# Kernel tuning notes

Measured on AMD Instinct MI355X. Metric: run time of the kernel, lower is better.

Reference implementation:

```python
import jax, jax.numpy as jnp
import numpy as np

B, P, F = 128, 196, 2048   # batch, num_pixels, feature_dim
E, H, V = 512, 512, 10000  # embed_dim, hidden_dim, vocab_size
T = 32                     # max caption length


def setup_inputs() -> dict:
    key = jax.random.key(0)
    ks = jax.random.split(key, 12)
    s_e, s_h, s_f = 1.0 / np.sqrt(E), 1.0 / np.sqrt(H), 1.0 / np.sqrt(F)
    return {
        "features": jax.random.normal(ks[0], (B, P, F), jnp.float32),
        "captions": jax.random.randint(ks[1], (B, T), 0, V),
        # embedding table (init uniform(-0.1, 0.1) in the original)
        "emb_W": jax.random.uniform(ks[2], (V, E), jnp.float32, -0.1, 0.1),
        # LSTMCell params (PyTorch layout: [4H, in] with gate order i,f,g,o)
        "W_ih": jax.random.uniform(ks[3], (4 * H, E), jnp.float32, -s_h, s_h),
        "W_hh": jax.random.uniform(ks[4], (4 * H, H), jnp.float32, -s_h, s_h),
        "b_ih": jax.random.uniform(ks[5], (4 * H,), jnp.float32, -s_h, s_h),
        "b_hh": jax.random.uniform(ks[6], (4 * H,), jnp.float32, -s_h, s_h),
        # init_h / init_c linear layers: feature_dim -> hidden_dim
        "Wh": jax.random.uniform(ks[7], (H, F), jnp.float32, -s_f, s_f),
        "bh": jax.random.uniform(ks[8], (H,), jnp.float32, -s_f, s_f),
        "Wc": jax.random.uniform(ks[9], (H, F), jnp.float32, -s_f, s_f),
        "bc": jax.random.uniform(ks[10], (H,), jnp.float32, -s_f, s_f),
        # output projection (uniform(-0.1, 0.1) weights, zero bias)
        "fc_W": jax.random.uniform(ks[11], (V, H), jnp.float32, -0.1, 0.1),
        "fc_b": jnp.zeros((V,), jnp.float32),
    }


def _decode(features, captions, emb_W, W_ih, W_hh, b_ih, b_hh, Wh, bh, Wc, bc, fc_W, fc_b):
    # init hidden state from mean pooled features
    mean_feat = features.mean(axis=1)                       # [B, F]
    h0 = mean_feat @ Wh.T + bh                              # [B, H]
    c0 = mean_feat @ Wc.T + bc                              # [B, H]

    embeds = emb_W[captions]                                # [B, T, E]
    # x-side gate preactivations for all steps at once: [T-1, B, 4H]
    x_gates = jnp.einsum('bte,ge->tbg', embeds[:, :-1, :], W_ih) + (b_ih + b_hh)

    def step(carry, xg):
        h, c = carry
        gates = xg + h @ W_hh.T                             # [B, 4H]
        i, f, g, o = jnp.split(gates, 4, axis=-1)
        i, f, o = jax.nn.sigmoid(i), jax.nn.sigmoid(f), jax.nn.sigmoid(o)
        g = jnp.tanh(g)
        c_new = f * c + i * g
        h_new = o * jnp.tanh(c_new)
        return (h_new, c_new), h_new

    _, hs = jax.lax.scan(step, (h0, c0), x_gates)           # hs: [T-1, B, H]
    hs = jnp.swapaxes(hs, 0, 1)                             # [B, T-1, H]
    # dropout is identity in eval mode; fc applied per step == batched matmul
    return jnp.einsum('bth,vh->btv', hs, fc_W) + fc_b       # [B, T-1, V]


def reference(features, captions, emb_W, W_ih, W_hh, b_ih, b_hh, Wh, bh, Wc, bc, fc_W, fc_b):
    return _decode(features, captions, emb_W, W_ih, W_hh, b_ih, b_hh, Wh, bh, Wc, bc, fc_W, fc_b)
```

## Files before the change

kernel.cpp:

```cpp
#include <hip/hip_runtime.h>
#include <hip/hip_bf16.h>
#include <cstddef>

#define Bz 128
#define Pz 196
#define Fz 2048
#define Ez 512
#define Hz 512
#define Vz 10000
#define Tz 32
#define TM 31
#define Mrows (Bz * TM)
#define G4 (4 * Hz)
#define NPAD 10112

typedef __attribute__((ext_vector_type(8))) short bf16x8;
typedef __attribute__((ext_vector_type(4))) float f32x4;

__device__ __forceinline__ void gload_lds16(const void* g, void* l) {
    __builtin_amdgcn_global_load_lds(
        (const __attribute__((address_space(1))) unsigned int*)g,
        (__attribute__((address_space(3))) unsigned int*)l, 16, 0, 0);
}
__device__ __forceinline__ ushort f2b(float x) {
    __hip_bfloat16 b = __float2bfloat16(x);
    return *reinterpret_cast<ushort*>(&b);
}
__device__ __forceinline__ float b2f(ushort u) {
    __hip_bfloat16 b = *reinterpret_cast<__hip_bfloat16*>(&u);
    return __bfloat162float(b);
}

__global__ __launch_bounds__(256) void meanpool(const float* __restrict__ feat,
                                                float* __restrict__ mean) {
    int idx = blockIdx.x * 256 + threadIdx.x;
    int b = idx >> 9;
    int q = idx & 511;
    const float4* base = reinterpret_cast<const float4*>(feat) +
                         (size_t)b * Pz * (Fz / 4) + q;
    float4 acc = {0.f, 0.f, 0.f, 0.f};
    for (int p = 0; p < Pz; ++p) {
        float4 v = base[(size_t)p * (Fz / 4)];
        acc.x += v.x; acc.y += v.y; acc.z += v.z; acc.w += v.w;
    }
    const float s = 1.0f / (float)Pz;
    acc.x *= s; acc.y *= s; acc.z *= s; acc.w *= s;
    reinterpret_cast<float4*>(mean)[idx] = acc;
}

__global__ __launch_bounds__(256) void gather_cvt_emb(const float* __restrict__ emb,
                                                      const int* __restrict__ cap,
                                                      ushort* __restrict__ out) {
    int idx = blockIdx.x * 256 + threadIdx.x;
    if (idx >= Mrows * (Ez / 4)) return;
    int m = idx >> 7, kq = idx & 127;
    int b = m / TM;
    int t = m - b * TM;
    int row = cap[b * Tz + t];
    float4 v = reinterpret_cast<const float4*>(emb + (size_t)row * Ez)[kq];
    ushort4 o = {f2b(v.x), f2b(v.y), f2b(v.z), f2b(v.w)};
    reinterpret_cast<ushort4*>(out + (size_t)m * Ez)[kq] = o;
}

__global__ __launch_bounds__(256) void permute_wih(const float* __restrict__ W,
                                                   const float* __restrict__ b1,
                                                   const float* __restrict__ b2,
                                                   ushort* __restrict__ WP,
                                                   float* __restrict__ bP) {
    int idx = blockIdx.x * 256 + threadIdx.x;
    int o = idx >> 7, kq = idx & 127;
    int j = o >> 2, g = o & 3;
    int in = g * Hz + j;
    float4 v = reinterpret_cast<const float4*>(W + (size_t)in * Ez)[kq];
    ushort4 u = {f2b(v.x), f2b(v.y), f2b(v.z), f2b(v.w)};
    reinterpret_cast<ushort4*>(WP + (size_t)o * Ez)[kq] = u;
    if (kq == 0) bP[o] = b1[in] + b2[in];
}

__global__ __launch_bounds__(256) void permute_whh(const float* __restrict__ W,
                                                   ushort* __restrict__ Whi) {
    int idx = blockIdx.x * 256 + threadIdx.x;
    int o = idx >> 7, kq = idx & 127;
    int j = o >> 2, g = o & 3;
    int in = g * Hz + j;
    float4 v = reinterpret_cast<const float4*>(W + (size_t)in * Hz)[kq];
    ushort4 h = {f2b(v.x), f2b(v.y), f2b(v.z), f2b(v.w)};
    reinterpret_cast<ushort4*>(Whi + (size_t)o * Hz)[kq] = h;
}

__global__ __launch_bounds__(256) void cvt_bf16_pad4(const float* __restrict__ s,
                                                     ushort* __restrict__ d,
                                                     int n4src, int n4dst) {
    int i = blockIdx.x * 256 + threadIdx.x;
    if (i >= n4dst) return;
    ushort4 o;
    if (i < n4src) {
        float4 v = reinterpret_cast<const float4*>(s)[i];
        o.x = f2b(v.x); o.y = f2b(v.y); o.z = f2b(v.z); o.w = f2b(v.w);
    } else {
        o.x = o.y = o.z = o.w = 0;
    }
    reinterpret_cast<ushort4*>(d)[i] = o;
}

__global__ __launch_bounds__(256) void initk(
    const float* __restrict__ mean,
    const float* __restrict__ Wh, const float* __restrict__ Wc,
    float* __restrict__ partial)
{
    __shared__ float As[64][33];
    __shared__ float Bs2[64][33];
    const int n0 = blockIdx.x * 64;
    const int m0 = blockIdx.y * 64;
    const int kz = blockIdx.z;
    const int tid = threadIdx.x;
    const int tx = tid & 15, ty = tid >> 4;
    float acc[4][4] = {};

    for (int k0 = kz * 256; k0 < kz * 256 + 256; k0 += 32) {
#pragma unroll
        for (int i = 0; i < 2; ++i) {
            int e  = tid + i * 256;
            int r  = e >> 3;
            int cc = (e & 7) << 2;
            float4 va = *reinterpret_cast<const float4*>(
                mean + (size_t)(m0 + r) * Fz + k0 + cc);
            As[r][cc + 0] = va.x; As[r][cc + 1] = va.y;
            As[r][cc + 2] = va.z; As[r][cc + 3] = va.w;
            int n = n0 + r;
            const float* Brow = (n < Hz) ? (Wh + (size_t)n * Fz)
                                         : (Wc + (size_t)(n - Hz) * Fz);
            float4 vb = *reinterpret_cast<const float4*>(Brow + k0 + cc);
            Bs2[r][cc + 0] = vb.x; Bs2[r][cc + 1] = vb.y;
            Bs2[r][cc + 2] = vb.z; Bs2[r][cc + 3] = vb.w;
        }
        __syncthreads();
#pragma unroll
        for (int kk = 0; kk < 32; ++kk) {
            float a[4], bb[4];
#pragma unroll
            for (int i = 0; i < 4; ++i) a[i] = As[ty * 4 + i][kk];
#pragma unroll
            for (int j = 0; j < 4; ++j) bb[j] = Bs2[tx * 4 + j][kk];
#pragma unroll
            for (int i = 0; i < 4; ++i)
#pragma unroll
                for (int j = 0; j < 4; ++j)
                    acc[i][j] += a[i] * bb[j];
        }
        __syncthreads();
    }
#pragma unroll
    for (int i = 0; i < 4; ++i)
#pragma unroll
        for (int j = 0; j < 4; ++j)
            partial[((size_t)kz * 128 + m0 + ty * 4 + i) * 1024 + n0 + tx * 4 + j]
                = acc[i][j];
}

__global__ __launch_bounds__(256) void init_reduce(
    const float* __restrict__ partial,
    const float* __restrict__ bh, const float* __restrict__ bc,
    ushort* __restrict__ haHi, ushort* __restrict__ haLo,
    float* __restrict__ c0f)
{
    int idx = blockIdx.x * 256 + threadIdx.x;
    if (idx >= 128 * 1024) return;
    int m = idx >> 10, n = idx & 1023;
    float s = 0.f;
#pragma unroll
    for (int z = 0; z < 8; ++z)
        s += partial[((size_t)z * 128 + m) * 1024 + n];
    if (n < Hz) {
        s += bh[n];
        ushort hh = f2b(s);
        haHi[(size_t)m * Hz + n] = hh;
        haLo[(size_t)m * Hz + n] = f2b(s - b2f(hh));
    } else {
        c0f[(size_t)m * Hz + (n - Hz)] = s + bc[n - Hz];
    }
}

__global__ __launch_bounds__(256) void gemm_mfma(
    const ushort* __restrict__ A,
    const ushort* __restrict__ B,
    const float* __restrict__ bias,
    float* __restrict__ C,
    int Nb, int ldc, int K)
{
    __shared__ short Al[2][128 * 32];
    __shared__ short Bl[2][128 * 32];
    const int tid  = threadIdx.x;
    const int w    = tid >> 6;
    const int lane = tid & 63;

    const int nwg  = gridDim.x * gridDim.y;
    int orig = blockIdx.y * gridDim.x + blockIdx.x;
    int q = nwg >> 3, r = nwg & 7;
    int xcd = orig & 7, local = orig >> 3;
    int wgid = (xcd < r ? xcd * (q + 1) : r * (q + 1) + (xcd - r) * q) + local;
    const int m0 = (wgid / gridDim.x) * 128;
    const int n0 = (wgid % gridDim.x) * 128;
    const int wr = w >> 1, wc = w & 1;

    f32x4 acc[4][4] = {};

    const int srow = w * 32 + (lane >> 2);
    const int scol = (lane & 3) * 16;
    const char* Ag = (const char*)(A + (size_t)(m0 + srow) * K) + scol;
    const char* Bg = (const char*)(B + (size_t)(n0 + srow) * K) + scol;
    const size_t rstep = (size_t)16 * K * 2;
    const int ldsb = (w * 32) * 32;

    const int ko = (lane >> 4) * 8;
    const int fr = lane & 15;
    const int nk = K >> 5;

    {
        gload_lds16(Ag,         Al[0] + ldsb);
        gload_lds16(Ag + rstep, Al[0] + ldsb + 16 * 32);
        gload_lds16(Bg,         Bl[0] + ldsb);
        gload_lds16(Bg + rstep, Bl[0] + ldsb + 16 * 32);
    }
    __syncthreads();

    int cur = 0;
    for (int k = 0; k < nk; ++k) {
        if (k + 1 < nk) {
            const size_t kb = (size_t)(k + 1) * 64;
            gload_lds16(Ag + kb,         Al[cur ^ 1] + ldsb);
            gload_lds16(Ag + kb + rstep, Al[cur ^ 1] + ldsb + 16 * 32);
            gload_lds16(Bg + kb,         Bl[cur ^ 1] + ldsb);
            gload_lds16(Bg + kb + rstep, Bl[cur ^ 1] + ldsb + 16 * 32);
        }
        bf16x8 af[4], bf[4];
#pragma unroll
        for (int i = 0; i < 4; ++i)
            af[i] = *reinterpret_cast<const bf16x8*>(&Al[cur][(wr * 64 + i * 16 + fr) * 32 + ko]);
#pragma unroll
        for (int j = 0; j < 4; ++j)
            bf[j] = *reinterpret_cast<const bf16x8*>(&Bl[cur][(wc * 64 + j * 16 + fr) * 32 + ko]);
#pragma unroll
        for (int i = 0; i < 4; ++i)
#pragma unroll
            for (int j = 0; j < 4; ++j)
                acc[i][j] = __builtin_amdgcn_mfma_f32_16x16x32_bf16(
                    af[i], bf[j], acc[i][j], 0, 0, 0);
        __syncthreads();
        cur ^= 1;
    }

    const int r0 = (lane >> 4) * 4;
#pragma unroll
    for (int i = 0; i < 4; ++i) {
        int row = m0 + wr * 64 + i * 16 + r0;
#pragma unroll
        for (int j = 0; j < 4; ++j) {
            int col = n0 + wc * 64 + j * 16 + fr;
            if (col < Nb) {
                float bb = bias ? bias[col] : 0.f;
#pragma unroll
                for (int rr = 0; rr < 4; ++rr)
                    C[(size_t)(row + rr) * ldc + col] = acc[i][j][rr] + bb;
            }
        }
    }
}

__global__ __launch_bounds__(64) void lstm_step2(
    const float* __restrict__ xg,
    const ushort* __restrict__ Whi,
    const ushort* __restrict__ Ah,  const ushort* __restrict__ Alo,
    ushort* __restrict__ Oh, ushort* __restrict__ Ol,
    float* __restrict__ cst, ushort* __restrict__ hsb, int t)
{
    __shared__ float Cl[32][17];

    const int tid  = threadIdx.x;
    const int lane = tid & 63;
    const int fr   = lane & 15;
    const int hi4  = lane >> 4;
    const int n0   = blockIdx.x * 16;
    const int j0   = n0 >> 2;
    const int m0w  = blockIdx.y * 32;

    f32x4 acc[2] = {};

    const ushort* Bp  = Whi + (size_t)(n0 + fr) * Hz;
    const ushort* Ap0 = Ah  + (size_t)(m0w + fr) * Hz;
    const ushort* Ap1 = Ah  + (size_t)(m0w + 16 + fr) * Hz;
    const ushort* Lp0 = Alo + (size_t)(m0w + fr) * Hz;
    const ushort* Lp1 = Alo + (size_t)(m0w + 16 + fr) * Hz;

#pragma unroll
    for (int kc = 0; kc < 16; ++kc) {
        const size_t koff = (size_t)kc * 32 + hi4 * 8;
        bf16x8 bv  = *reinterpret_cast<const bf16x8*>(Bp  + koff);
        bf16x8 ah0 = *reinterpret_cast<const bf16x8*>(Ap0 + koff);
        bf16x8 ah1 = *reinterpret_cast<const bf16x8*>(Ap1 + koff);
        bf16x8 al0 = *reinterpret_cast<const bf16x8*>(Lp0 + koff);
        bf16x8 al1 = *reinterpret_cast<const bf16x8*>(Lp1 + koff);
        acc[0] = __builtin_amdgcn_mfma_f32_16x16x32_bf16(ah0, bv, acc[0], 0, 0, 0);
        acc[1] = __builtin_amdgcn_mfma_f32_16x16x32_bf16(ah1, bv, acc[1], 0, 0, 0);
        acc[0] = __builtin_amdgcn_mfma_f32_16x16x32_bf16(al0, bv, acc[0], 0, 0, 0);
        acc[1] = __builtin_amdgcn_mfma_f32_16x16x32_bf16(al1, bv, acc[1], 0, 0, 0);
    }

#pragma unroll
    for (int i = 0; i < 2; ++i)
#pragma unroll
        for (int r = 0; r < 4; ++r)
            Cl[i * 16 + hi4 * 4 + r][fr] = acc[i][r];
    __syncthreads();

    {
        const int lm = tid >> 1;
        const int m  = m0w + lm;
        const int hp = (tid & 1) * 2;
        const float* xr = xg + ((size_t)m * TM + t) * G4 + n0 + 4 * hp;
        float4 x0 = *reinterpret_cast<const float4*>(xr);
        float4 x1 = *reinterpret_cast<const float4*>(xr + 4);
        float2 cc = *reinterpret_cast<const float2*>(cst + (size_t)m * Hz + j0 + hp);

        float gi0 = Cl[lm][4 * hp + 0] + x0.x;
        float gf0 = Cl[lm][4 * hp + 1] + x0.y;
        float gg0 = Cl[lm][4 * hp + 2] + x0.z;
        float go0 = Cl[lm][4 * hp + 3] + x0.w;
        float gi1 = Cl[lm][4 * hp + 4] + x1.x;
        float gf1 = Cl[lm][4 * hp + 5] + x1.y;
        float gg1 = Cl[lm][4 * hp + 6] + x1.z;
        float go1 = Cl[lm][4 * hp + 7] + x1.w;

        float i0 = 1.f / (1.f + expf(-gi0));
        float f0 = 1.f / (1.f + expf(-gf0));
        float g0 = tanhf(gg0);
        float o0 = 1.f / (1.f + expf(-go0));
        float i1 = 1.f / (1.f + expf(-gi1));
        float f1 = 1.f / (1.f + expf(-gf1));
        float g1 = tanhf(gg1);
        float o1 = 1.f / (1.f + expf(-go1));

        float cn0 = f0 * cc.x + i0 * g0;
        float cn1 = f1 * cc.y + i1 * g1;
        float h0v = o0 * tanhf(cn0);
        float h1v = o1 * tanhf(cn1);

        float2 cno = {cn0, cn1};
        *reinterpret_cast<float2*>(cst + (size_t)m * Hz + j0 + hp) = cno;

        ushort hh0 = f2b(h0v), hh1 = f2b(h1v);
        ushort hl0 = f2b(h0v - b2f(hh0)), hl1 = f2b(h1v - b2f(hh1));
        uint uh = (uint)hh0 | ((uint)hh1 << 16);
        uint ul = (uint)hl0 | ((uint)hl1 << 16);
        *reinterpret_cast<uint*>(Oh + (size_t)m * Hz + j0 + hp) = uh;
        *reinterpret_cast<uint*>(Ol + (size_t)m * Hz + j0 + hp) = ul;
        *reinterpret_cast<uint*>(hsb + ((size_t)m * TM + t) * Hz + j0 + hp) = uh;
    }
}

extern "C" void kernel_launch(void* const* d_in, const int* in_sizes, int n_in,
                              void* d_out, int out_size, void* d_ws, size_t ws_size,
                              hipStream_t stream) {
    const float* features = (const float*)d_in[0];
    const int*   captions = (const int*)d_in[1];
    const float* emb_W    = (const float*)d_in[2];
    const float* W_ih     = (const float*)d_in[3];
    const float* W_hh     = (const float*)d_in[4];
    const float* b_ih     = (const float*)d_in[5];
    const float* b_hh     = (const float*)d_in[6];
    const float* Wh       = (const float*)d_in[7];
    const float* bh       = (const float*)d_in[8];
    const float* Wc       = (const float*)d_in[9];
    const float* bc       = (const float*)d_in[10];
    const float* fc_W     = (const float*)d_in[11];
    const float* fc_b     = (const float*)d_in[12];
    float* out = (float*)d_out;

    float* w    = (float*)d_ws;
    float* mean = w;
    float* xg   = mean + Bz * Fz;
    float* partial = xg;
    float* c0f  = xg + (size_t)Mrows * G4;
    float* bP   = c0f + Bz * Hz;
    ushort* embg = (ushort*)(bP + G4);
    ushort* WihP = embg + (size_t)Mrows * Ez;
    ushort* Whi  = WihP + (size_t)G4 * Ez;
    ushort* fcWb = Whi + (size_t)G4 * Hz;
    ushort* hsb  = fcWb + (size_t)NPAD * Hz;
    ushort* haHi = hsb + (size_t)Mrows * Hz;
    ushort* haLo = haHi + Bz * Hz;
    ushort* hbHi = haLo + Bz * Hz;
    ushort* hbLo = hbHi + Bz * Hz;

    meanpool<<<(Bz * Fz / 4) / 256, 256, 0, stream>>>(features, mean);
    gather_cvt_emb<<<(Mrows * (Ez / 4) + 255) / 256, 256, 0, stream>>>(emb_W, captions, embg);
    permute_wih<<<(G4 * (Ez / 4)) / 256, 256, 0, stream>>>(W_ih, b_ih, b_hh, WihP, bP);
    permute_whh<<<(G4 * (Hz / 4)) / 256, 256, 0, stream>>>(W_hh, Whi);
    cvt_bf16_pad4<<<(NPAD * Hz / 4 + 255) / 256, 256, 0, stream>>>(
        fc_W, fcWb, Vz * Hz / 4, NPAD * Hz / 4);

    initk<<<dim3(16, 2, 8), 256, 0, stream>>>(mean, Wh, Wc, partial);
    init_reduce<<<(128 * 1024) / 256, 256, 0, stream>>>(
        partial, bh, bc, haHi, haLo, c0f);

    gemm_mfma<<<dim3(G4 / 128, Mrows / 128), 256, 0, stream>>>(
        embg, WihP, bP, xg, G4, G4, Ez);

    for (int t = 0; t < TM; ++t) {
        const ushort* ih = (t & 1) ? hbHi : haHi;
        const ushort* il = (t & 1) ? hbLo : haLo;
        ushort* oh = (t & 1) ? haHi : hbHi;
        ushort* ol = (t & 1) ? haLo : hbLo;
        lstm_step2<<<dim3(G4 / 16, 4), 64, 0, stream>>>(
            xg, Whi, ih, il, oh, ol, c0f, hsb, t);
    }

    gemm_mfma<<<dim3(NPAD / 128, Mrows / 128), 256, 0, stream>>>(
        hsb, fcWb, fc_b, out, Vz, Vz, Hz);
}
```

Baseline: 482.1 us.

## Add B-stationary fc GEMM, widen LSTM step blocks, merge weight permute kernels

Swaps the final vocab projection onto a new kernel. Each 512-thread block keeps a 64-column slice of fc weights (full K=512) resident in swizzled LDS and walks up to 8 row tiles, streaming A from global memory. The LSTM step kernel now uses two waves per block covering 32 gate columns, halving the grid. The two weight-permute kernels are merged into one launch. The aim is less launch overhead and better B reuse in the dominant output GEMM. The risks are lower occupancy from 64KB of LDS per block, and A reads from global memory with no LDS staging.

```diff
diff --git a/kernel.cpp b/kernel.cpp
--- a/kernel.cpp
+++ b/kernel.cpp
@@ -62,30 +62,27 @@
     reinterpret_cast<ushort4*>(out + (size_t)m * Ez)[kq] = o;
 }
 
-__global__ __launch_bounds__(256) void permute_wih(const float* __restrict__ W,
-                                                   const float* __restrict__ b1,
-                                                   const float* __restrict__ b2,
-                                                   ushort* __restrict__ WP,
-                                                   float* __restrict__ bP) {
+__global__ __launch_bounds__(256) void permute_w(
+    const float* __restrict__ Wih, const float* __restrict__ Whh,
+    const float* __restrict__ b1,  const float* __restrict__ b2,
+    ushort* __restrict__ WihP, ushort* __restrict__ WhhP,
+    float* __restrict__ bP) {
     int idx = blockIdx.x * 256 + threadIdx.x;
-    int o = idx >> 7, kq = idx & 127;
+    int sel = idx >> 18;
+    int rem = idx & ((1 << 18) - 1);
+    int o = rem >> 7, kq = rem & 127;
     int j = o >> 2, g = o & 3;
     int in = g * Hz + j;
-    float4 v = reinterpret_cast<const float4*>(W + (size_t)in * Ez)[kq];
-    ushort4 u = {f2b(v.x), f2b(v.y), f2b(v.z), f2b(v.w)};
-    reinterpret_cast<ushort4*>(WP + (size_t)o * Ez)[kq] = u;
-    if (kq == 0) bP[o] = b1[in] + b2[in];
-}
-
-__global__ __launch_bounds__(256) void permute_whh(const float* __restrict__ W,
-                                                   ushort* __restrict__ Whi) {
-    int idx = blockIdx.x * 256 + threadIdx.x;
-    int o = idx >> 7, kq = idx & 127;
-    int j = o >> 2, g = o & 3;
-    int in = g * Hz + j;
-    float4 v = reinterpret_cast<const float4*>(W + (size_t)in * Hz)[kq];
-    ushort4 h = {f2b(v.x), f2b(v.y), f2b(v.z), f2b(v.w)};
-    reinterpret_cast<ushort4*>(Whi + (size_t)o * Hz)[kq] = h;
+    if (sel == 0) {
+        float4 v = reinterpret_cast<const float4*>(Wih + (size_t)in * Ez)[kq];
+        ushort4 u = {f2b(v.x), f2b(v.y), f2b(v.z), f2b(v.w)};
+        reinterpret_cast<ushort4*>(WihP + (size_t)o * Ez)[kq] = u;
+        if (kq == 0) bP[o] = b1[in] + b2[in];
+    } else {
+        float4 v = reinterpret_cast<const float4*>(Whh + (size_t)in * Hz)[kq];
+        ushort4 u = {f2b(v.x), f2b(v.y), f2b(v.z), f2b(v.w)};
+        reinterpret_cast<ushort4*>(WhhP + (size_t)o * Hz)[kq] = u;
+    }
 }
 
 __global__ __launch_bounds__(256) void cvt_bf16_pad4(const float* __restrict__ s,
@@ -216,12 +213,10 @@
     const int fr = lane & 15;
     const int nk = K >> 5;
 
-    {
-        gload_lds16(Ag,         Al[0] + ldsb);
-        gload_lds16(Ag + rstep, Al[0] + ldsb + 16 * 32);
-        gload_lds16(Bg,         Bl[0] + ldsb);
-        gload_lds16(Bg + rstep, Bl[0] + ldsb + 16 * 32);
-    }
+    gload_lds16(Ag,         Al[0] + ldsb);
+    gload_lds16(Ag + rstep, Al[0] + ldsb + 16 * 32);
+    gload_lds16(Bg,         Bl[0] + ldsb);
+    gload_lds16(Bg + rstep, Bl[0] + ldsb + 16 * 32);
     __syncthreads();
 
     int cur = 0;
@@ -267,26 +262,96 @@
     }
 }
 
-__global__ __launch_bounds__(64) void lstm_step2(
+__global__ __launch_bounds__(512) void fc_gemm(
+    const ushort* __restrict__ A,
+    const ushort* __restrict__ B,
+    const float* __restrict__ bias,
+    float* __restrict__ C)
+{
+    __shared__ short Bl[64 * 512];
+    const int tid  = threadIdx.x;
+    const int w    = tid >> 6;
+    const int lane = tid & 63;
+    const int fr   = lane & 15;
+    const int hi4  = lane >> 4;
+    const int n0   = blockIdx.x * 64;
+    const int by   = blockIdx.y;
+
+    for (int i = 0; i < 8; ++i) {
+        int n = w * 8 + i;
+        const ushort* src = B + (size_t)(n0 + n) * Hz + (size_t)((lane ^ (n & 7)) * 8);
+        gload_lds16(src, (char*)Bl + n * 1024);
+    }
+    __syncthreads();
+
+    const int wm = w >> 1;
+    const int nl = (w & 1) * 32;
+
+    for (int i = 0; i < 8; ++i) {
+        int mt = by * 8 + i;
+        if (mt >= 31) break;
+        const int m0 = mt * 128 + wm * 32;
+        f32x4 acc[2][2] = {};
+        const ushort* Ap0 = A + (size_t)(m0 + fr) * Hz;
+        const ushort* Ap1 = A + (size_t)(m0 + 16 + fr) * Hz;
+        const int nA = nl + fr;
+        const int nB = nl + 16 + fr;
+        const char* BpA = (const char*)Bl + nA * 1024;
+        const char* BpB = (const char*)Bl + nB * 1024;
+        const int sxA = (nA & 7) << 4;
+        const int sxB = (nB & 7) << 4;
+#pragma unroll
+        for (int kc = 0; kc < 16; ++kc) {
+            const int koff = kc * 32 + hi4 * 8;
+            const int pb   = (koff << 1);
+            bf16x8 a0 = *reinterpret_cast<const bf16x8*>(Ap0 + koff);
+            bf16x8 a1 = *reinterpret_cast<const bf16x8*>(Ap1 + koff);
+            bf16x8 b0 = *reinterpret_cast<const bf16x8*>(BpA + (pb ^ sxA));
+            bf16x8 b1 = *reinterpret_cast<const bf16x8*>(BpB + (pb ^ sxB));
+            acc[0][0] = __builtin_amdgcn_mfma_f32_16x16x32_bf16(a0, b0, acc[0][0], 0, 0, 0);
+            acc[0][1] = __builtin_amdgcn_mfma_f32_16x16x32_bf16(a0, b1, acc[0][1], 0, 0, 0);
+            acc[1][0] = __builtin_amdgcn_mfma_f32_16x16x32_bf16(a1, b0, acc[1][0], 0, 0, 0);
+            acc[1][1] = __builtin_amdgcn_mfma_f32_16x16x32_bf16(a1, b1, acc[1][1], 0, 0, 0);
+        }
+        const int r0 = hi4 * 4;
+#pragma unroll
+        for (int ii = 0; ii < 2; ++ii) {
+            int row = m0 + ii * 16 + r0;
+#pragma unroll
+            for (int j = 0; j < 2; ++j) {
+                int col = n0 + nl + j * 16 + fr;
+                if (col < Vz) {
+                    float bb = bias[col];
+#pragma unroll
+                    for (int rr = 0; rr < 4; ++rr)
+                        C[(size_t)(row + rr) * Vz + col] = acc[ii][j][rr] + bb;
+                }
+            }
+        }
+    }
+}
+
+__global__ __launch_bounds__(128) void lstm_step2(
     const float* __restrict__ xg,
     const ushort* __restrict__ Whi,
     const ushort* __restrict__ Ah,  const ushort* __restrict__ Alo,
     ushort* __restrict__ Oh, ushort* __restrict__ Ol,
     float* __restrict__ cst, ushort* __restrict__ hsb, int t)
 {
-    __shared__ float Cl[32][17];
+    __shared__ float Cl[32][33];
 
     const int tid  = threadIdx.x;
+    const int w    = tid >> 6;
     const int lane = tid & 63;
     const int fr   = lane & 15;
     const int hi4  = lane >> 4;
-    const int n0   = blockIdx.x * 16;
-    const int j0   = n0 >> 2;
+    const int n0   = blockIdx.x * 32;
+    const int j0   = blockIdx.x * 8;
     const int m0w  = blockIdx.y * 32;
 
     f32x4 acc[2] = {};
 
-    const ushort* Bp  = Whi + (size_t)(n0 + fr) * Hz;
+    const ushort* Bp  = Whi + (size_t)(n0 + w * 16 + fr) * Hz;
     const ushort* Ap0 = Ah  + (size_t)(m0w + fr) * Hz;
     const ushort* Ap1 = Ah  + (size_t)(m0w + 16 + fr) * Hz;
     const ushort* Lp0 = Alo + (size_t)(m0w + fr) * Hz;
@@ -310,26 +375,27 @@
     for (int i = 0; i < 2; ++i)
 #pragma unroll
         for (int r = 0; r < 4; ++r)
-            Cl[i * 16 + hi4 * 4 + r][fr] = acc[i][r];
+            Cl[i * 16 + hi4 * 4 + r][w * 16 + fr] = acc[i][r];
     __syncthreads();
 
     {
-        const int lm = tid >> 1;
+        const int lm = tid >> 2;
         const int m  = m0w + lm;
-        const int hp = (tid & 1) * 2;
-        const float* xr = xg + ((size_t)m * TM + t) * G4 + n0 + 4 * hp;
+        const int bc = (tid & 3) * 8;
+        const float* xr = xg + ((size_t)m * TM + t) * G4 + n0 + bc;
         float4 x0 = *reinterpret_cast<const float4*>(xr);
         float4 x1 = *reinterpret_cast<const float4*>(xr + 4);
-        float2 cc = *reinterpret_cast<const float2*>(cst + (size_t)m * Hz + j0 + hp);
-
-        float gi0 = Cl[lm][4 * hp + 0] + x0.x;
-        float gf0 = Cl[lm][4 * hp + 1] + x0.y;
-        float gg0 = Cl[lm][4 * hp + 2] + x0.z;
-        float go0 = Cl[lm][4 * hp + 3] + x0.w;
-        float gi1 = Cl[lm][4 * hp + 4] + x1.x;
-        float gf1 = Cl[lm][4 * hp + 5] + x1.y;
-        float gg1 = Cl[lm][4 * hp + 6] + x1.z;
-        float go1 = Cl[lm][4 * hp + 7] + x1.w;
+        const int jj = j0 + (tid & 3) * 2;
+        float2 cc = *reinterpret_cast<const float2*>(cst + (size_t)m * Hz + jj);
+
+        float gi0 = Cl[lm][bc + 0] + x0.x;
+        float gf0 = Cl[lm][bc + 1] + x0.y;
+        float gg0 = Cl[lm][bc + 2] + x0.z;
+        float go0 = Cl[lm][bc + 3] + x0.w;
+        float gi1 = Cl[lm][bc + 4] + x1.x;
+        float gf1 = Cl[lm][bc + 5] + x1.y;
+        float gg1 = Cl[lm][bc + 6] + x1.z;
+        float go1 = Cl[lm][bc + 7] + x1.w;
 
         float i0 = 1.f / (1.f + expf(-gi0));
         float f0 = 1.f / (1.f + expf(-gf0));
@@ -346,15 +412,15 @@
         float h1v = o1 * tanhf(cn1);
 
         float2 cno = {cn0, cn1};
-        *reinterpret_cast<float2*>(cst + (size_t)m * Hz + j0 + hp) = cno;
+        *reinterpret_cast<float2*>(cst + (size_t)m * Hz + jj) = cno;
 
         ushort hh0 = f2b(h0v), hh1 = f2b(h1v);
         ushort hl0 = f2b(h0v - b2f(hh0)), hl1 = f2b(h1v - b2f(hh1));
         uint uh = (uint)hh0 | ((uint)hh1 << 16);
         uint ul = (uint)hl0 | ((uint)hl1 << 16);
-        *reinterpret_cast<uint*>(Oh + (size_t)m * Hz + j0 + hp) = uh;
-        *reinterpret_cast<uint*>(Ol + (size_t)m * Hz + j0 + hp) = ul;
-        *reinterpret_cast<uint*>(hsb + ((size_t)m * TM + t) * Hz + j0 + hp) = uh;
+        *reinterpret_cast<uint*>(Oh + (size_t)m * Hz + jj) = uh;
+        *reinterpret_cast<uint*>(Ol + (size_t)m * Hz + jj) = ul;
+        *reinterpret_cast<uint*>(hsb + ((size_t)m * TM + t) * Hz + jj) = uh;
     }
 }
 
@@ -394,8 +460,8 @@
 
     meanpool<<<(Bz * Fz / 4) / 256, 256, 0, stream>>>(features, mean);
     gather_cvt_emb<<<(Mrows * (Ez / 4) + 255) / 256, 256, 0, stream>>>(emb_W, captions, embg);
-    permute_wih<<<(G4 * (Ez / 4)) / 256, 256, 0, stream>>>(W_ih, b_ih, b_hh, WihP, bP);
-    permute_whh<<<(G4 * (Hz / 4)) / 256, 256, 0, stream>>>(W_hh, Whi);
+    permute_w<<<(2 * G4 * (Hz / 4)) / 256, 256, 0, stream>>>(
+        W_ih, W_hh, b_ih, b_hh, WihP, Whi, bP);
     cvt_bf16_pad4<<<(NPAD * Hz / 4 + 255) / 256, 256, 0, stream>>>(
         fc_W, fcWb, Vz * Hz / 4, NPAD * Hz / 4);
 
@@ -411,10 +477,9 @@
         const ushort* il = (t & 1) ? hbLo : haLo;
         ushort* oh = (t & 1) ? haHi : hbHi;
         ushort* ol = (t & 1) ? haLo : hbLo;
-        lstm_step2<<<dim3(G4 / 16, 4), 64, 0, stream>>>(
+        lstm_step2<<<dim3(64, 4), 128, 0, stream>>>(
             xg, Whi, ih, il, oh, ol, c0f, hsb, t);
     }
 
-    gemm_mfma<<<dim3(NPAD / 128, Mrows / 128), 256, 0, stream>>>(
-        hsb, fcWb, fc_b, out, Vz, Vz, Hz);
-}
+    fc_gemm<<<dim3(NPAD / 64, 4), 512, 0, stream>>>(hsb, fcWb, fc_b, out);
+}
```

Result: slower. 585.7 us (+21.5%).
